# Performance work log

Measured on AMD Instinct MI355X. Metric: run time of the kernel, lower is better.

Reference implementation:

```python
import jax, jax.numpy as jnp
import numpy as np

B, S, D = 4, 2048, 1024
H = 16
HD = D // H  # 64

def setup_inputs() -> dict:
    key = jax.random.key(0)
    ks = jax.random.split(key, 4)
    scale = 0.02
    return {
        "hidden_states": jax.random.normal(ks[0], (B, S, D), dtype=jnp.float32),
        "attention_mask": jnp.zeros((B, 1, 1, S), dtype=jnp.float32),
        "Wq": jax.random.normal(ks[1], (D, D), dtype=jnp.float32) * scale,
        "bq": jnp.zeros((D,), dtype=jnp.float32),
        "Wk": jax.random.normal(ks[2], (D, D), dtype=jnp.float32) * scale,
        "bk": jnp.zeros((D,), dtype=jnp.float32),
        "Wv": jax.random.normal(ks[3], (D, D), dtype=jnp.float32) * scale,
        "bv": jnp.zeros((D,), dtype=jnp.float32),
    }

def reference(hidden_states, attention_mask, Wq, bq, Wk, bk, Wv, bv):
    b, s, d = hidden_states.shape
    def proj(W, bias):
        # Linear then split heads: [b, s, d] -> [b, H, s, HD]
        y = hidden_states @ W.T + bias
        return y.reshape(b, s, H, HD).transpose(0, 2, 1, 3)
    Q = proj(Wq, bq)
    K = proj(Wk, bk)
    V = proj(Wv, bv)
    scores = jnp.einsum('bhqd,bhkd->bhqk', Q, K) / jnp.sqrt(jnp.float32(HD))
    scores = scores + attention_mask  # additive mask, broadcast [b,1,1,s]
    probs = jax.nn.softmax(scores, axis=-1)
    # dropout prob = 0.0 (eval-mode): identity
    context = jnp.einsum('bhqk,bhkd->bhqd', probs, V)
    return context.transpose(0, 2, 1, 3).reshape(b, s, d)
```

## Files before the change

kernel.cpp:

```cpp
#include <hip/hip_runtime.h>


typedef short bf16x4 __attribute__((ext_vector_type(4)));
typedef short bf16x8 __attribute__((ext_vector_type(8)));
typedef float f32x4 __attribute__((ext_vector_type(4)));

#define SEQ 2048
#define DIM 1024
#define NH 16
#define HDIM 64
#define QKV_ELEMS ((size_t)64 * SEQ * HDIM)

#define WS_FLAG  50331648ull
#define WS_XBF   50331904ull
#define WS_WBF   67109120ull
#define WS_BF32  73400576ull
#define WS_NEED  73412868ull

#define LOG2E 1.4426950408889634f
#define QSCALE (0.125f * LOG2E)

static __device__ __forceinline__ unsigned short f2bf(float f) {
  union { float f; unsigned u; } x; x.f = f;
  unsigned r = x.u + 0x7fffu + ((x.u >> 16) & 1u);
  return (unsigned short)(r >> 16);
}
static __device__ __forceinline__ float bf2f(unsigned short h) {
  union { unsigned u; float f; } x; x.u = ((unsigned)h) << 16;
  return x.f;
}
static __device__ __forceinline__ unsigned pk2bf(float a, float b) {
  union { float f; unsigned u; } x, y; x.f = a; y.f = b;
  return __builtin_amdgcn_perm(y.u + 0x8000u, x.u + 0x8000u, 0x07060302u);
}
static __device__ __forceinline__ int vswz(int s) {
  return (s & ~31) | (((s >> 2) & 3) << 3) | (((s >> 4) & 1) << 2);
}

template <bool FP32>
static __device__ __forceinline__ float load1(const void* p, size_t i) {
  if (FP32) return ((const float*)p)[i];
  else      return bf2f(((const unsigned short*)p)[i]);
}
template <bool FP32>
static __device__ __forceinline__ bf16x8 load8bf(const void* p, size_t i) {
  if (FP32) {
    f32x4 a = *(const f32x4*)((const float*)p + i);
    f32x4 b = *(const f32x4*)((const float*)p + i + 4);
    union { bf16x8 v; unsigned short u[8]; } r;
#pragma unroll
    for (int j = 0; j < 4; ++j) { r.u[j] = f2bf(a[j]); r.u[4 + j] = f2bf(b[j]); }
    return r.v;
  } else {
    return *(const bf16x8*)((const unsigned short*)p + i);
  }
}

static __device__ __forceinline__ void glds16(const unsigned short* g, unsigned short* l) {
  __builtin_amdgcn_global_load_lds(
      (const __attribute__((address_space(1))) unsigned int*)(unsigned long long)(const void*)g,
      (__attribute__((address_space(3))) unsigned int*)(unsigned int)(unsigned long long)(void*)l,
      16, 0, 0);
}

__global__ void detect_dtype(const unsigned short* __restrict__ X, int* __restrict__ flag) {
  __shared__ int zc[256], bc[256];
  int z = 0, b = 0;
  for (int i = threadIdx.x; i < 16384; i += 256) {
    unsigned short u = X[2 * i];
    if (u == 0) z++;
    int e = (u >> 7) & 0xff;
    if (e >= 134) b++;
  }
  zc[threadIdx.x] = z; bc[threadIdx.x] = b;
  __syncthreads();
  for (int s = 128; s > 0; s >>= 1) {
    if (threadIdx.x < s) { zc[threadIdx.x] += zc[threadIdx.x + s]; bc[threadIdx.x] += bc[threadIdx.x + s]; }
    __syncthreads();
  }
  if (threadIdx.x == 0)
    *flag = (zc[0] > 8192 || bc[0] > 64) ? 1 : 0;
}

template <bool FP32>
__global__ void convert_all(const void* __restrict__ X,
                            const void* __restrict__ Wq, const void* __restrict__ Wk,
                            const void* __restrict__ Wv,
                            const void* __restrict__ bq, const void* __restrict__ bk,
                            const void* __restrict__ bv,
                            unsigned char* __restrict__ ws, const int* __restrict__ flag) {
  if (*flag != (FP32 ? 1 : 0)) return;
  unsigned short* Xb = (unsigned short*)(ws + WS_XBF);
  unsigned short* Wb = (unsigned short*)(ws + WS_WBF);
  float* Bb = (float*)(ws + WS_BF32);
  int blk = blockIdx.x;
  if (blk < 4096) {
    size_t base = ((size_t)blk * 256 + threadIdx.x) * 8;
    *(bf16x8*)(Xb + base) = load8bf<FP32>(X, base);
  } else if (blk < 5632) {
    int w = (blk - 4096) >> 9;
    int r = (blk - 4096) & 511;
    const void* W = (w == 0) ? Wq : (w == 1) ? Wk : Wv;
    size_t base = ((size_t)r * 256 + threadIdx.x) * 8;
    *(bf16x8*)(Wb + (size_t)w * 1048576 + base) = load8bf<FP32>(W, base);
  } else {
    int w = blk - 5632;
    const void* Bsrc = (w == 0) ? bq : (w == 1) ? bk : bv;
    for (int i = threadIdx.x; i < 1024; i += 256)
      Bb[w * 1024 + i] = load1<FP32>(Bsrc, i);
  }
}

#define XS_STRIDE 40
__global__ __launch_bounds__(256) void qkv_bf(
    const unsigned short* __restrict__ Xb, const unsigned short* __restrict__ Wb,
    const float* __restrict__ Bb,
    unsigned short* __restrict__ Qo, unsigned short* __restrict__ Ko,
    unsigned short* __restrict__ Vo)
{
  const int z = blockIdx.z;
  const unsigned short* W = Wb + (size_t)z * 1048576;

  __shared__ __align__(16) unsigned short Xs[128 * XS_STRIDE];
  __shared__ __align__(16) unsigned short Ws[128 * XS_STRIDE];

  const int tid  = threadIdx.x;
  const int wave = tid >> 6;
  const int lane = tid & 63;
  const int col  = lane & 15;
  const int quad = lane >> 4;
  const int wr = wave & 1;
  const int wc = wave >> 1;
  const int m0 = blockIdx.x * 128;
  const int n0 = blockIdx.y * 128;

  f32x4 zero4 = {0.f, 0.f, 0.f, 0.f};
  f32x4 acc[4][4];
#pragma unroll
  for (int i = 0; i < 4; ++i)
#pragma unroll
    for (int j = 0; j < 4; ++j) acc[i][j] = zero4;

  const int srow = tid >> 2;
  const int sseg = (tid & 3) << 3;

  for (int k0 = 0; k0 < DIM; k0 += 32) {
    __syncthreads();
#pragma unroll
    for (int a = 0; a < 2; ++a) {
      int r = a * 64 + srow;
      *(bf16x8*)(Xs + r * XS_STRIDE + sseg) = *(const bf16x8*)(Xb + (size_t)(m0 + r) * DIM + k0 + sseg);
      *(bf16x8*)(Ws + r * XS_STRIDE + sseg) = *(const bf16x8*)(W  + (size_t)(n0 + r) * DIM + k0 + sseg);
    }
    __syncthreads();

    bf16x8 Af[4], Bf[4];
#pragma unroll
    for (int i = 0; i < 4; ++i)
      Af[i] = *(const bf16x8*)(Xs + (wr * 64 + i * 16 + col) * XS_STRIDE + quad * 8);
#pragma unroll
    for (int j = 0; j < 4; ++j)
      Bf[j] = *(const bf16x8*)(Ws + (wc * 64 + j * 16 + col) * XS_STRIDE + quad * 8);
#pragma unroll
    for (int i = 0; i < 4; ++i)
#pragma unroll
      for (int j = 0; j < 4; ++j)
        acc[i][j] = __builtin_amdgcn_mfma_f32_16x16x32_bf16(Af[i], Bf[j], acc[i][j], 0, 0, 0);
  }

  const float oscale = (z == 0) ? QSCALE : 1.0f;
  if (z < 2) {
    unsigned short* Yo = (z == 0) ? Qo : Ko;
#pragma unroll
    for (int i = 0; i < 4; ++i) {
#pragma unroll
      for (int j = 0; j < 4; ++j) {
        int n = n0 + wc * 64 + j * 16 + col;
        float bvf = Bb[z * 1024 + n];
        int h = n >> 6, hd = n & 63;
#pragma unroll
        for (int r = 0; r < 4; ++r) {
          int m = m0 + wr * 64 + i * 16 + quad * 4 + r;
          int b = m >> 11, s = m & 2047;
          Yo[((size_t)(b * NH + h) * SEQ + s) * HDIM + hd] = f2bf((acc[i][j][r] + bvf) * oscale);
        }
      }
    }
  } else {
#pragma unroll
    for (int i = 0; i < 4; ++i) {
#pragma unroll
      for (int j = 0; j < 4; ++j) {
        int n = n0 + wc * 64 + j * 16 + col;
        float bvf = Bb[2 * 1024 + n];
        int h = n >> 6, hd = n & 63;
        int mbase = m0 + wr * 64 + i * 16 + quad * 4;
        int b = mbase >> 11, s = mbase & 2047;
        unsigned long long pk = 0;
#pragma unroll
        for (int r = 0; r < 4; ++r)
          pk |= (unsigned long long)f2bf(acc[i][j][r] + bvf) << (16 * r);
        *(unsigned long long*)(Vo + ((size_t)(b * NH + h) * HDIM + hd) * SEQ + vswz(s)) = pk;
      }
    }
  }
}

template <bool FP32>
__global__ __launch_bounds__(256) void qkv_any(
    const void* __restrict__ X,
    const void* __restrict__ Wq, const void* __restrict__ bq,
    const void* __restrict__ Wk, const void* __restrict__ bk,
    const void* __restrict__ Wv, const void* __restrict__ bv,
    unsigned short* __restrict__ Qo, unsigned short* __restrict__ Ko,
    unsigned short* __restrict__ Vo, const int* __restrict__ flag)
{
  if (*flag != (FP32 ? 1 : 0)) return;
  const int z = blockIdx.z;
  const void* W    = (z == 0) ? Wq : (z == 1) ? Wk : Wv;
  const void* bias = (z == 0) ? bq : (z == 1) ? bk : bv;

  __shared__ __align__(16) unsigned short Xs[128 * XS_STRIDE];
  __shared__ __align__(16) unsigned short Ws[128 * XS_STRIDE];

  const int tid  = threadIdx.x;
  const int wave = tid >> 6;
  const int lane = tid & 63;
  const int col  = lane & 15;
  const int quad = lane >> 4;
  const int wr = wave & 1;
  const int wc = wave >> 1;
  const int m0 = blockIdx.x * 128;
  const int n0 = blockIdx.y * 128;

  f32x4 zero4 = {0.f, 0.f, 0.f, 0.f};
  f32x4 acc[4][4];
#pragma unroll
  for (int i = 0; i < 4; ++i)
#pragma unroll
    for (int j = 0; j < 4; ++j) acc[i][j] = zero4;

  const int srow = tid >> 2;
  const int sseg = (tid & 3) << 3;

  for (int k0 = 0; k0 < DIM; k0 += 32) {
    __syncthreads();
#pragma unroll
    for (int a = 0; a < 2; ++a) {
      int r = a * 64 + srow;
      *(bf16x8*)(Xs + r * XS_STRIDE + sseg) = load8bf<FP32>(X, (size_t)(m0 + r) * DIM + k0 + sseg);
      *(bf16x8*)(Ws + r * XS_STRIDE + sseg) = load8bf<FP32>(W, (size_t)(n0 + r) * DIM + k0 + sseg);
    }
    __syncthreads();

    bf16x8 Af[4], Bf[4];
#pragma unroll
    for (int i = 0; i < 4; ++i)
      Af[i] = *(const bf16x8*)(Xs + (wr * 64 + i * 16 + col) * XS_STRIDE + quad * 8);
#pragma unroll
    for (int j = 0; j < 4; ++j)
      Bf[j] = *(const bf16x8*)(Ws + (wc * 64 + j * 16 + col) * XS_STRIDE + quad * 8);
#pragma unroll
    for (int i = 0; i < 4; ++i)
#pragma unroll
      for (int j = 0; j < 4; ++j)
        acc[i][j] = __builtin_amdgcn_mfma_f32_16x16x32_bf16(Af[i], Bf[j], acc[i][j], 0, 0, 0);
  }

  const float oscale = (z == 0) ? QSCALE : 1.0f;
  if (z < 2) {
    unsigned short* Yo = (z == 0) ? Qo : Ko;
#pragma unroll
    for (int i = 0; i < 4; ++i) {
#pragma unroll
      for (int j = 0; j < 4; ++j) {
        int n = n0 + wc * 64 + j * 16 + col;
        float bvf = load1<FP32>(bias, n);
        int h = n >> 6, hd = n & 63;
#pragma unroll
        for (int r = 0; r < 4; ++r) {
          int m = m0 + wr * 64 + i * 16 + quad * 4 + r;
          int b = m >> 11, s = m & 2047;
          Yo[((size_t)(b * NH + h) * SEQ + s) * HDIM + hd] = f2bf((acc[i][j][r] + bvf) * oscale);
        }
      }
    }
  } else {
#pragma unroll
    for (int i = 0; i < 4; ++i) {
#pragma unroll
      for (int j = 0; j < 4; ++j) {
        int n = n0 + wc * 64 + j * 16 + col;
        float bvf = load1<FP32>(bias, n);
        int h = n >> 6, hd = n & 63;
        int mbase = m0 + wr * 64 + i * 16 + quad * 4;
        int b = mbase >> 11, s = mbase & 2047;
        unsigned long long pk = 0;
#pragma unroll
        for (int r = 0; r < 4; ++r)
          pk |= (unsigned long long)f2bf(acc[i][j][r] + bvf) << (16 * r);
        *(unsigned long long*)(Vo + ((size_t)(b * NH + h) * HDIM + hd) * SEQ + vswz(s)) = pk;
      }
    }
  }
}

template <bool FP32>
__global__ __launch_bounds__(256, 4) void attn_kernel(
    const unsigned short* __restrict__ Q,
    const unsigned short* __restrict__ K,
    const unsigned short* __restrict__ Vt,
    const void* __restrict__ mask,
    void* __restrict__ OutV, const int* __restrict__ flag)
{
  if (*flag != (FP32 ? 1 : 0)) return;

  __shared__ __align__(16) unsigned short Ks[128 * 64];
  __shared__ __align__(16) unsigned short Vs[64 * 128];
  __shared__ __align__(16) float Ms[128];

  const int tid  = threadIdx.x;
  const int wave = tid >> 6;
  const int lane = tid & 63;
  const int col  = lane & 15;
  const int quad = lane >> 4;
  const int qt = blockIdx.x;
  const int bh = blockIdx.y;
  const int b  = bh >> 4;
  const int h  = bh & 15;

  const unsigned short* Qb = Q  + (size_t)bh * SEQ * HDIM;
  const unsigned short* Kb = K  + (size_t)bh * SEQ * HDIM;
  const unsigned short* Vb = Vt + (size_t)bh * HDIM * SEQ;

  const int qrow = qt * 64 + wave * 16 + col;
  const bf16x8 Qf0 = *(const bf16x8*)(Qb + (size_t)qrow * HDIM + quad * 8);
  const bf16x8 Qf1 = *(const bf16x8*)(Qb + (size_t)qrow * HDIM + 32 + quad * 8);

  const f32x4 z4 = {0.f, 0.f, 0.f, 0.f};
  f32x4 Oacc[4];
  f32x4 Osum = z4;
#pragma unroll
  for (int t = 0; t < 4; ++t) Oacc[t] = z4;
  float mrun = -1e30f;

  union { bf16x8 v; unsigned u[4]; } ones;
#pragma unroll
  for (int i = 0; i < 4; ++i) ones.u[i] = 0x3F803F80u;

  const int krow_in = lane >> 3;
  const int kphys   = lane & 7;
  const int vrow_in = lane >> 4;
  const int vphys   = lane & 15;

  for (int kt = 0; kt < 16; ++kt) {
    __syncthreads();
    {
#pragma unroll
      for (int a = 0; a < 4; ++a) {
        int row = wave * 32 + a * 8 + krow_in;
        int lseg = kphys ^ (row & 7);
        glds16(Kb + (size_t)(kt * 128 + row) * HDIM + lseg * 8,
               Ks + (wave * 32 + a * 8) * 64);
      }
#pragma unroll
      for (int a = 0; a < 4; ++a) {
        int row = wave * 16 + a * 4 + vrow_in;
        int lseg = vphys ^ (row & 15);
        glds16(Vb + (size_t)row * SEQ + kt * 128 + lseg * 8,
               Vs + (wave * 16 + a * 4) * 128);
      }
      if (tid < 128)
        Ms[tid] = load1<FP32>(mask, (size_t)b * SEQ + kt * 128 + tid) * LOG2E;
    }
    __syncthreads();

    f32x4 st[8];
#pragma unroll
    for (int t = 0; t < 8; ++t) {
      const unsigned short* kr = Ks + (t * 16 + col) * 64;
      bf16x8 Ka = *(const bf16x8*)(kr + (quad ^ (col & 7)) * 8);
      bf16x8 Kc = *(const bf16x8*)(kr + ((4 + quad) ^ (col & 7)) * 8);
      f32x4 d = *(const f32x4*)(Ms + t * 16 + quad * 4);
      d = __builtin_amdgcn_mfma_f32_16x16x32_bf16(Ka, Qf0, d, 0, 0, 0);
      d = __builtin_amdgcn_mfma_f32_16x16x32_bf16(Kc, Qf1, d, 0, 0, 0);
      st[t] = d;
    }

    f32x4 m4 = st[0];
#pragma unroll
    for (int t = 1; t < 8; ++t)
#pragma unroll
      for (int r = 0; r < 4; ++r) m4[r] = fmaxf(m4[r], st[t][r]);
    float pm = fmaxf(fmaxf(m4[0], m4[1]), fmaxf(m4[2], m4[3]));
    pm = fmaxf(pm, __shfl_xor(pm, 16, 64));
    pm = fmaxf(pm, __shfl_xor(pm, 32, 64));
    float mn = fmaxf(mrun, pm);
    float alpha = __builtin_amdgcn_exp2f(mrun - mn);
    mrun = mn;
#pragma unroll
    for (int t = 0; t < 8; ++t)
#pragma unroll
      for (int r = 0; r < 4; ++r) st[t][r] = __builtin_amdgcn_exp2f(st[t][r] - mn);

    float av[4];
#pragma unroll
    for (int r = 0; r < 4; ++r) av[r] = __shfl(alpha, quad * 4 + r, 64);
#pragma unroll
    for (int t = 0; t < 4; ++t)
#pragma unroll
      for (int r = 0; r < 4; ++r) Oacc[t][r] *= av[r];
#pragma unroll
    for (int r = 0; r < 4; ++r) Osum[r] *= av[r];

#pragma unroll
    for (int tp = 0; tp < 4; ++tp) {
      union { bf16x8 v; unsigned u[4]; } Af;
      Af.u[0] = pk2bf(st[2 * tp][0],     st[2 * tp][1]);
      Af.u[1] = pk2bf(st[2 * tp][2],     st[2 * tp][3]);
      Af.u[2] = pk2bf(st[2 * tp + 1][0], st[2 * tp + 1][1]);
      Af.u[3] = pk2bf(st[2 * tp + 1][2], st[2 * tp + 1][3]);
      Osum = __builtin_amdgcn_mfma_f32_16x16x32_bf16(Af.v, ones.v, Osum, 0, 0, 0);
#pragma unroll
      for (int t2 = 0; t2 < 4; ++t2) {
        bf16x8 Bv = *(const bf16x8*)(Vs + (t2 * 16 + col) * 128 + ((tp * 4 + quad) ^ col) * 8);
        Oacc[t2] = __builtin_amdgcn_mfma_f32_16x16x32_bf16(Af.v, Bv, Oacc[t2], 0, 0, 0);
      }
    }
  }

  float liv[4];
#pragma unroll
  for (int r = 0; r < 4; ++r) liv[r] = 1.0f / Osum[r];
#pragma unroll
  for (int t2 = 0; t2 < 4; ++t2) {
#pragma unroll
    for (int r = 0; r < 4; ++r) {
      int q = qt * 64 + wave * 16 + quad * 4 + r;
      float v = Oacc[t2][r] * liv[r];
      v = (v == v) ? v : 0.0f;
      size_t oidx = ((size_t)b * SEQ + q) * DIM + h * HDIM + t2 * 16 + col;
      if (FP32) ((float*)OutV)[oidx] = v;
      else      ((unsigned short*)OutV)[oidx] = f2bf(v);
    }
  }
}

extern "C" void kernel_launch(void* const* d_in, const int* in_sizes, int n_in,
                              void* d_out, int out_size, void* d_ws, size_t ws_size,
                              hipStream_t stream) {
  const void* X    = d_in[0];
  const void* mask = d_in[1];
  const void* Wq   = d_in[2];
  const void* bq   = d_in[3];
  const void* Wk   = d_in[4];
  const void* bk   = d_in[5];
  const void* Wv   = d_in[6];
  const void* bv   = d_in[7];

  unsigned char* ws = (unsigned char*)d_ws;
  unsigned short* Qw = (unsigned short*)ws;
  unsigned short* Kw = Qw + QKV_ELEMS;
  unsigned short* Vw = Kw + QKV_ELEMS;
  int* flag = (int*)(ws + WS_FLAG);

  detect_dtype<<<1, 256, 0, stream>>>((const unsigned short*)X, flag);

  if (ws_size >= WS_NEED) {
    convert_all<false><<<5635, 256, 0, stream>>>(X, Wq, Wk, Wv, bq, bk, bv, ws, flag);
    convert_all<true ><<<5635, 256, 0, stream>>>(X, Wq, Wk, Wv, bq, bk, bv, ws, flag);
    qkv_bf<<<dim3(64, 8, 3), 256, 0, stream>>>(
        (const unsigned short*)(ws + WS_XBF), (const unsigned short*)(ws + WS_WBF),
        (const float*)(ws + WS_BF32), Qw, Kw, Vw);
  } else {
    qkv_any<false><<<dim3(64, 8, 3), 256, 0, stream>>>(X, Wq, bq, Wk, bk, Wv, bv, Qw, Kw, Vw, flag);
    qkv_any<true ><<<dim3(64, 8, 3), 256, 0, stream>>>(X, Wq, bq, Wk, bk, Wv, bv, Qw, Kw, Vw, flag);
  }

  attn_kernel<false><<<dim3(32, 64), 256, 0, stream>>>(Qw, Kw, Vw, mask, d_out, flag);
  attn_kernel<true ><<<dim3(32, 64), 256, 0, stream>>>(Qw, Kw, Vw, mask, d_out, flag);
}
```

Measured before the change: 304.3 us.

## Double-buffer attention K/V, double queries per wave, lazy rescale, async GEMM loads

The attention kernel now double-buffers K/V tiles in LDS so the next tile's global-to-LDS copy overlaps compute. Each wave handles 32 query rows instead of 16, halving the grid and reusing each K/V fragment twice. The whole mask row is preloaded once per block, and the running-max rescale is skipped while the max grows by at most 8 (log2 units). The QKV GEMM switches to 64-wide K steps with swizzled direct global-to-LDS loads. The costs are more registers and LDS, occupancy lowered to 2 blocks per CU, and fewer blocks in flight.

```diff
diff --git a/kernel.cpp b/kernel.cpp
--- a/kernel.cpp
+++ b/kernel.cpp
@@ -111,7 +111,6 @@
   }
 }
 
-#define XS_STRIDE 40
 __global__ __launch_bounds__(256) void qkv_bf(
     const unsigned short* __restrict__ Xb, const unsigned short* __restrict__ Wb,
     const float* __restrict__ Bb,
@@ -121,8 +120,8 @@
   const int z = blockIdx.z;
   const unsigned short* W = Wb + (size_t)z * 1048576;
 
-  __shared__ __align__(16) unsigned short Xs[128 * XS_STRIDE];
-  __shared__ __align__(16) unsigned short Ws[128 * XS_STRIDE];
+  __shared__ __align__(16) unsigned short Xs[128 * 64];
+  __shared__ __align__(16) unsigned short Ws[128 * 64];
 
   const int tid  = threadIdx.x;
   const int wave = tid >> 6;
@@ -141,31 +140,37 @@
 #pragma unroll
     for (int j = 0; j < 4; ++j) acc[i][j] = zero4;
 
-  const int srow = tid >> 2;
-  const int sseg = (tid & 3) << 3;
-
-  for (int k0 = 0; k0 < DIM; k0 += 32) {
+  const int srow8 = lane >> 3;
+  const int sseg  = lane & 7;
+
+  for (int k0 = 0; k0 < DIM; k0 += 64) {
     __syncthreads();
 #pragma unroll
-    for (int a = 0; a < 2; ++a) {
-      int r = a * 64 + srow;
-      *(bf16x8*)(Xs + r * XS_STRIDE + sseg) = *(const bf16x8*)(Xb + (size_t)(m0 + r) * DIM + k0 + sseg);
-      *(bf16x8*)(Ws + r * XS_STRIDE + sseg) = *(const bf16x8*)(W  + (size_t)(n0 + r) * DIM + k0 + sseg);
+    for (int a = 0; a < 4; ++a) {
+      int rowbase = wave * 32 + a * 8;
+      int row = rowbase + srow8;
+      int lseg = sseg ^ (row & 7);
+      glds16(Xb + (size_t)(m0 + row) * DIM + k0 + lseg * 8, Xs + rowbase * 64);
+      glds16(W  + (size_t)(n0 + row) * DIM + k0 + lseg * 8, Ws + rowbase * 64);
     }
     __syncthreads();
 
-    bf16x8 Af[4], Bf[4];
-#pragma unroll
-    for (int i = 0; i < 4; ++i)
-      Af[i] = *(const bf16x8*)(Xs + (wr * 64 + i * 16 + col) * XS_STRIDE + quad * 8);
-#pragma unroll
-    for (int j = 0; j < 4; ++j)
-      Bf[j] = *(const bf16x8*)(Ws + (wc * 64 + j * 16 + col) * XS_STRIDE + quad * 8);
-#pragma unroll
-    for (int i = 0; i < 4; ++i)
-#pragma unroll
-      for (int j = 0; j < 4; ++j)
-        acc[i][j] = __builtin_amdgcn_mfma_f32_16x16x32_bf16(Af[i], Bf[j], acc[i][j], 0, 0, 0);
+#pragma unroll
+    for (int kk = 0; kk < 2; ++kk) {
+      bf16x8 Af[4], Bf[4];
+#pragma unroll
+      for (int i = 0; i < 4; ++i) {
+        int ra = wr * 64 + i * 16 + col;
+        Af[i] = *(const bf16x8*)(Xs + ra * 64 + ((kk * 4 + quad) ^ (ra & 7)) * 8);
+        int rb = wc * 64 + i * 16 + col;
+        Bf[i] = *(const bf16x8*)(Ws + rb * 64 + ((kk * 4 + quad) ^ (rb & 7)) * 8);
+      }
+#pragma unroll
+      for (int i = 0; i < 4; ++i)
+#pragma unroll
+        for (int j = 0; j < 4; ++j)
+          acc[i][j] = __builtin_amdgcn_mfma_f32_16x16x32_bf16(Af[i], Bf[j], acc[i][j], 0, 0, 0);
+    }
   }
 
   const float oscale = (z == 0) ? QSCALE : 1.0f;
@@ -206,6 +211,7 @@
   }
 }
 
+#define XS_STRIDE 40
 template <bool FP32>
 __global__ __launch_bounds__(256) void qkv_any(
     const void* __restrict__ X,
@@ -306,7 +312,7 @@
 }
 
 template <bool FP32>
-__global__ __launch_bounds__(256, 4) void attn_kernel(
+__global__ __launch_bounds__(256, 2) void attn_kernel(
     const unsigned short* __restrict__ Q,
     const unsigned short* __restrict__ K,
     const unsigned short* __restrict__ Vt,
@@ -315,9 +321,9 @@
 {
   if (*flag != (FP32 ? 1 : 0)) return;
 
-  __shared__ __align__(16) unsigned short Ks[128 * 64];
-  __shared__ __align__(16) unsigned short Vs[64 * 128];
-  __shared__ __align__(16) float Ms[128];
+  __shared__ __align__(16) unsigned short Ks[2 * 128 * 64];
+  __shared__ __align__(16) unsigned short Vs[2 * 64 * 128];
+  __shared__ __align__(16) float Msall[SEQ];
 
   const int tid  = threadIdx.x;
   const int wave = tid >> 6;
@@ -333,16 +339,36 @@
   const unsigned short* Kb = K  + (size_t)bh * SEQ * HDIM;
   const unsigned short* Vb = Vt + (size_t)bh * HDIM * SEQ;
 
-  const int qrow = qt * 64 + wave * 16 + col;
-  const bf16x8 Qf0 = *(const bf16x8*)(Qb + (size_t)qrow * HDIM + quad * 8);
-  const bf16x8 Qf1 = *(const bf16x8*)(Qb + (size_t)qrow * HDIM + 32 + quad * 8);
+  if (FP32) {
+    const float* mp = (const float*)mask + (size_t)b * SEQ + tid * 8;
+    f32x4 a = *(const f32x4*)mp;
+    f32x4 c = *(const f32x4*)(mp + 4);
+#pragma unroll
+    for (int j = 0; j < 4; ++j) {
+      Msall[tid * 8 + j]     = a[j] * LOG2E;
+      Msall[tid * 8 + 4 + j] = c[j] * LOG2E;
+    }
+  } else {
+    const unsigned short* mp = (const unsigned short*)mask + (size_t)b * SEQ + tid * 8;
+    bf16x8 v = *(const bf16x8*)mp;
+#pragma unroll
+    for (int j = 0; j < 8; ++j)
+      Msall[tid * 8 + j] = bf2f((unsigned short)v[j]) * LOG2E;
+  }
+
+  const int qrow0 = qt * 128 + wave * 32 + col;
+  const int qrow1 = qrow0 + 16;
+  const bf16x8 Qf00 = *(const bf16x8*)(Qb + (size_t)qrow0 * HDIM + quad * 8);
+  const bf16x8 Qf01 = *(const bf16x8*)(Qb + (size_t)qrow0 * HDIM + 32 + quad * 8);
+  const bf16x8 Qf10 = *(const bf16x8*)(Qb + (size_t)qrow1 * HDIM + quad * 8);
+  const bf16x8 Qf11 = *(const bf16x8*)(Qb + (size_t)qrow1 * HDIM + 32 + quad * 8);
 
   const f32x4 z4 = {0.f, 0.f, 0.f, 0.f};
-  f32x4 Oacc[4];
-  f32x4 Osum = z4;
-#pragma unroll
-  for (int t = 0; t < 4; ++t) Oacc[t] = z4;
-  float mrun = -1e30f;
+  f32x4 Oacc0[4], Oacc1[4];
+  f32x4 Osum0 = z4, Osum1 = z4;
+#pragma unroll
+  for (int t = 0; t < 4; ++t) { Oacc0[t] = z4; Oacc1[t] = z4; }
+  float mrun0 = -1e30f, mrun1 = -1e30f;
 
   union { bf16x8 v; unsigned u[4]; } ones;
 #pragma unroll
@@ -353,95 +379,139 @@
   const int vrow_in = lane >> 4;
   const int vphys   = lane & 15;
 
+  auto stage = [&](int ktn, int bufn) {
+    unsigned short* Kdst = Ks + bufn * (128 * 64);
+    unsigned short* Vdst = Vs + bufn * (64 * 128);
+#pragma unroll
+    for (int a = 0; a < 4; ++a) {
+      int row = wave * 32 + a * 8 + krow_in;
+      int lseg = kphys ^ (row & 7);
+      glds16(Kb + (size_t)(ktn * 128 + row) * HDIM + lseg * 8,
+             Kdst + (wave * 32 + a * 8) * 64);
+    }
+#pragma unroll
+    for (int a = 0; a < 4; ++a) {
+      int row = wave * 16 + a * 4 + vrow_in;
+      int lseg = vphys ^ (row & 15);
+      glds16(Vb + (size_t)row * SEQ + ktn * 128 + lseg * 8,
+             Vdst + (wave * 16 + a * 4) * 128);
+    }
+  };
+
+  stage(0, 0);
+
   for (int kt = 0; kt < 16; ++kt) {
     __syncthreads();
-    {
-#pragma unroll
-      for (int a = 0; a < 4; ++a) {
-        int row = wave * 32 + a * 8 + krow_in;
-        int lseg = kphys ^ (row & 7);
-        glds16(Kb + (size_t)(kt * 128 + row) * HDIM + lseg * 8,
-               Ks + (wave * 32 + a * 8) * 64);
-      }
-#pragma unroll
-      for (int a = 0; a < 4; ++a) {
-        int row = wave * 16 + a * 4 + vrow_in;
-        int lseg = vphys ^ (row & 15);
-        glds16(Vb + (size_t)row * SEQ + kt * 128 + lseg * 8,
-               Vs + (wave * 16 + a * 4) * 128);
-      }
-      if (tid < 128)
-        Ms[tid] = load1<FP32>(mask, (size_t)b * SEQ + kt * 128 + tid) * LOG2E;
-    }
-    __syncthreads();
-
-    f32x4 st[8];
+    if (kt < 15) stage(kt + 1, (kt + 1) & 1);
+
+    const unsigned short* Kcur = Ks + (kt & 1) * (128 * 64);
+    const unsigned short* Vcur = Vs + (kt & 1) * (64 * 128);
+    const float* Mc = Msall + kt * 128;
+
+    f32x4 st0[8], st1[8];
 #pragma unroll
     for (int t = 0; t < 8; ++t) {
-      const unsigned short* kr = Ks + (t * 16 + col) * 64;
+      const unsigned short* kr = Kcur + (t * 16 + col) * 64;
       bf16x8 Ka = *(const bf16x8*)(kr + (quad ^ (col & 7)) * 8);
       bf16x8 Kc = *(const bf16x8*)(kr + ((4 + quad) ^ (col & 7)) * 8);
-      f32x4 d = *(const f32x4*)(Ms + t * 16 + quad * 4);
-      d = __builtin_amdgcn_mfma_f32_16x16x32_bf16(Ka, Qf0, d, 0, 0, 0);
-      d = __builtin_amdgcn_mfma_f32_16x16x32_bf16(Kc, Qf1, d, 0, 0, 0);
-      st[t] = d;
-    }
-
-    f32x4 m4 = st[0];
+      f32x4 c = *(const f32x4*)(Mc + t * 16 + quad * 4);
+      f32x4 d0 = c, d1 = c;
+      d0 = __builtin_amdgcn_mfma_f32_16x16x32_bf16(Ka, Qf00, d0, 0, 0, 0);
+      d0 = __builtin_amdgcn_mfma_f32_16x16x32_bf16(Kc, Qf01, d0, 0, 0, 0);
+      d1 = __builtin_amdgcn_mfma_f32_16x16x32_bf16(Ka, Qf10, d1, 0, 0, 0);
+      d1 = __builtin_amdgcn_mfma_f32_16x16x32_bf16(Kc, Qf11, d1, 0, 0, 0);
+      st0[t] = d0; st1[t] = d1;
+    }
+
+    f32x4 m40 = st0[0], m41 = st1[0];
 #pragma unroll
     for (int t = 1; t < 8; ++t)
 #pragma unroll
-      for (int r = 0; r < 4; ++r) m4[r] = fmaxf(m4[r], st[t][r]);
-    float pm = fmaxf(fmaxf(m4[0], m4[1]), fmaxf(m4[2], m4[3]));
-    pm = fmaxf(pm, __shfl_xor(pm, 16, 64));
-    pm = fmaxf(pm, __shfl_xor(pm, 32, 64));
-    float mn = fmaxf(mrun, pm);
-    float alpha = __builtin_amdgcn_exp2f(mrun - mn);
-    mrun = mn;
+      for (int r = 0; r < 4; ++r) {
+        m40[r] = fmaxf(m40[r], st0[t][r]);
+        m41[r] = fmaxf(m41[r], st1[t][r]);
+      }
+    float pm0 = fmaxf(fmaxf(m40[0], m40[1]), fmaxf(m40[2], m40[3]));
+    float pm1 = fmaxf(fmaxf(m41[0], m41[1]), fmaxf(m41[2], m41[3]));
+    pm0 = fmaxf(pm0, __shfl_xor(pm0, 16, 64));
+    pm0 = fmaxf(pm0, __shfl_xor(pm0, 32, 64));
+    pm1 = fmaxf(pm1, __shfl_xor(pm1, 16, 64));
+    pm1 = fmaxf(pm1, __shfl_xor(pm1, 32, 64));
+
+    if (!__all((pm0 - mrun0 <= 8.0f) && (pm1 - mrun1 <= 8.0f))) {
+      float mn0 = fmaxf(mrun0, pm0), mn1 = fmaxf(mrun1, pm1);
+      float a0 = __builtin_amdgcn_exp2f(mrun0 - mn0);
+      float a1 = __builtin_amdgcn_exp2f(mrun1 - mn1);
+      mrun0 = mn0; mrun1 = mn1;
+      float av0[4], av1[4];
+#pragma unroll
+      for (int r = 0; r < 4; ++r) {
+        av0[r] = __shfl(a0, quad * 4 + r, 64);
+        av1[r] = __shfl(a1, quad * 4 + r, 64);
+      }
+#pragma unroll
+      for (int t = 0; t < 4; ++t)
+#pragma unroll
+        for (int r = 0; r < 4; ++r) {
+          Oacc0[t][r] *= av0[r];
+          Oacc1[t][r] *= av1[r];
+        }
+#pragma unroll
+      for (int r = 0; r < 4; ++r) { Osum0[r] *= av0[r]; Osum1[r] *= av1[r]; }
+    }
+
 #pragma unroll
     for (int t = 0; t < 8; ++t)
 #pragma unroll
-      for (int r = 0; r < 4; ++r) st[t][r] = __builtin_amdgcn_exp2f(st[t][r] - mn);
-
-    float av[4];
-#pragma unroll
-    for (int r = 0; r < 4; ++r) av[r] = __shfl(alpha, quad * 4 + r, 64);
-#pragma unroll
-    for (int t = 0; t < 4; ++t)
-#pragma unroll
-      for (int r = 0; r < 4; ++r) Oacc[t][r] *= av[r];
-#pragma unroll
-    for (int r = 0; r < 4; ++r) Osum[r] *= av[r];
+      for (int r = 0; r < 4; ++r) {
+        st0[t][r] = __builtin_amdgcn_exp2f(st0[t][r] - mrun0);
+        st1[t][r] = __builtin_amdgcn_exp2f(st1[t][r] - mrun1);
+      }
 
 #pragma unroll
     for (int tp = 0; tp < 4; ++tp) {
-      union { bf16x8 v; unsigned u[4]; } Af;
-      Af.u[0] = pk2bf(st[2 * tp][0],     st[2 * tp][1]);
-      Af.u[1] = pk2bf(st[2 * tp][2],     st[2 * tp][3]);
-      Af.u[2] = pk2bf(st[2 * tp + 1][0], st[2 * tp + 1][1]);
-      Af.u[3] = pk2bf(st[2 * tp + 1][2], st[2 * tp + 1][3]);
-      Osum = __builtin_amdgcn_mfma_f32_16x16x32_bf16(Af.v, ones.v, Osum, 0, 0, 0);
+      union { bf16x8 v; unsigned u[4]; } A0, A1;
+      A0.u[0] = pk2bf(st0[2 * tp][0],     st0[2 * tp][1]);
+      A0.u[1] = pk2bf(st0[2 * tp][2],     st0[2 * tp][3]);
+      A0.u[2] = pk2bf(st0[2 * tp + 1][0], st0[2 * tp + 1][1]);
+      A0.u[3] = pk2bf(st0[2 * tp + 1][2], st0[2 * tp + 1][3]);
+      A1.u[0] = pk2bf(st1[2 * tp][0],     st1[2 * tp][1]);
+      A1.u[1] = pk2bf(st1[2 * tp][2],     st1[2 * tp][3]);
+      A1.u[2] = pk2bf(st1[2 * tp + 1][0], st1[2 * tp + 1][1]);
+      A1.u[3] = pk2bf(st1[2 * tp + 1][2], st1[2 * tp + 1][3]);
+      Osum0 = __builtin_amdgcn_mfma_f32_16x16x32_bf16(A0.v, ones.v, Osum0, 0, 0, 0);
+      Osum1 = __builtin_amdgcn_mfma_f32_16x16x32_bf16(A1.v, ones.v, Osum1, 0, 0, 0);
 #pragma unroll
       for (int t2 = 0; t2 < 4; ++t2) {
-        bf16x8 Bv = *(const bf16x8*)(Vs + (t2 * 16 + col) * 128 + ((tp * 4 + quad) ^ col) * 8);
-        Oacc[t2] = __builtin_amdgcn_mfma_f32_16x16x32_bf16(Af.v, Bv, Oacc[t2], 0, 0, 0);
-      }
-    }
-  }
-
-  float liv[4];
-#pragma unroll
-  for (int r = 0; r < 4; ++r) liv[r] = 1.0f / Osum[r];
+        bf16x8 Bv = *(const bf16x8*)(Vcur + (t2 * 16 + col) * 128 + ((tp * 4 + quad) ^ col) * 8);
+        Oacc0[t2] = __builtin_amdgcn_mfma_f32_16x16x32_bf16(A0.v, Bv, Oacc0[t2], 0, 0, 0);
+        Oacc1[t2] = __builtin_amdgcn_mfma_f32_16x16x32_bf16(A1.v, Bv, Oacc1[t2], 0, 0, 0);
+      }
+    }
+  }
+
+  float liv0[4], liv1[4];
+#pragma unroll
+  for (int r = 0; r < 4; ++r) { liv0[r] = 1.0f / Osum0[r]; liv1[r] = 1.0f / Osum1[r]; }
 #pragma unroll
   for (int t2 = 0; t2 < 4; ++t2) {
 #pragma unroll
     for (int r = 0; r < 4; ++r) {
-      int q = qt * 64 + wave * 16 + quad * 4 + r;
-      float v = Oacc[t2][r] * liv[r];
-      v = (v == v) ? v : 0.0f;
-      size_t oidx = ((size_t)b * SEQ + q) * DIM + h * HDIM + t2 * 16 + col;
-      if (FP32) ((float*)OutV)[oidx] = v;
-      else      ((unsigned short*)OutV)[oidx] = f2bf(v);
+      int q0 = qt * 128 + wave * 32 + quad * 4 + r;
+      int q1 = q0 + 16;
+      float v0 = Oacc0[t2][r] * liv0[r];
+      float v1 = Oacc1[t2][r] * liv1[r];
+      v0 = (v0 == v0) ? v0 : 0.0f;
+      v1 = (v1 == v1) ? v1 : 0.0f;
+      size_t o0 = ((size_t)b * SEQ + q0) * DIM + h * HDIM + t2 * 16 + col;
+      size_t o1 = ((size_t)b * SEQ + q1) * DIM + h * HDIM + t2 * 16 + col;
+      if (FP32) {
+        ((float*)OutV)[o0] = v0;
+        ((float*)OutV)[o1] = v1;
+      } else {
+        ((unsigned short*)OutV)[o0] = f2bf(v0);
+        ((unsigned short*)OutV)[o1] = f2bf(v1);
+      }
     }
   }
 }
@@ -477,6 +547,6 @@
     qkv_any<true ><<<dim3(64, 8, 3), 256, 0, stream>>>(X, Wq, bq, Wk, bk, Wv, bv, Qw, Kw, Vw, flag);
   }
 
-  attn_kernel<false><<<dim3(32, 64), 256, 0, stream>>>(Qw, Kw, Vw, mask, d_out, flag);
-  attn_kernel<true ><<<dim3(32, 64), 256, 0, stream>>>(Qw, Kw, Vw, mask, d_out, flag);
-}
+  attn_kernel<false><<<dim3(16, 64), 256, 0, stream>>>(Qw, Kw, Vw, mask, d_out, flag);
+  attn_kernel<true ><<<dim3(16, 64), 256, 0, stream>>>(Qw, Kw, Vw, mask, d_out, flag);
+}
```

After: 269.8 us. 1.13x faster.
